# Kernel optimization log

Hardware: AMD Instinct MI355X
Metric: run time of the kernel (lower is better)

## Reference

```python
import jax, jax.numpy as jnp
import numpy as np


def dht(x):
    # Discrete Hartley transform over spatial dims via FFT (ortho norm):
    # H(x) = Re(F(x)) - Im(F(x)). With norm='ortho' the DHT is its own inverse.
    X = jnp.fft.fftn(x, axes=(2, 3), norm='ortho')
    return X.real - X.imag


def _neg_freq(a):
    # H[-k] = roll(flip(H), 1) along both spectral dims
    return jnp.roll(jnp.flip(a, axis=(-2, -1)), shift=(1, 1), axis=(-2, -1))


def compl_mul2d(x1, x2):
    x1n = _neg_freq(x1)
    x2n = _neg_freq(x2)
    return 0.5 * (
        jnp.einsum('bixy,ioxy->boxy', x1, x2)
        - jnp.einsum('bixy,ioxy->boxy', x1n, x2n)
        + jnp.einsum('bixy,ioxy->boxy', x1, x2n)
        + jnp.einsum('bixy,ioxy->boxy', x1n, x2)
    )


def setup_inputs() -> dict:
    key = jax.random.key(0)
    k1, k2 = jax.random.split(key)
    B, Ci, Co, S, M = 16, 32, 32, 256, 16
    x = jax.random.normal(k1, (B, Ci, S, S), dtype=jnp.float32)
    scale = 1.0 / (Ci * Co)
    weights1 = scale * jax.random.uniform(k2, (Ci, Co, M, M), dtype=jnp.float32)
    return {'x': x, 'weights1': weights1}


def reference(x, weights1):
    B = x.shape[0]
    S1, S2 = x.shape[-2], x.shape[-1]
    Co = weights1.shape[1]
    m1, m2 = weights1.shape[2], weights1.shape[3]
    x_ht = dht(x)                                   # [B, Ci, S1, S2]
    res = compl_mul2d(x_ht[:, :, :m1, :m2], weights1)  # [B, Co, m1, m2]
    out_ht = jnp.zeros((B, Co, S1, S2), dtype=x.dtype).at[:, :, :m1, :m2].set(res)
    return dht(out_ht)                              # inverse DHT == DHT (ortho)
```

## Files before the change

kernel.cpp:

```cpp
#include <hip/hip_runtime.h>

#define CI 32
#define CO 32

constexpr float INV_S = 1.0f / 256.0f;
constexpr float THETA = 6.28318530717958647692f / 256.0f;

__device__ constexpr float RC[16] = {
  1.0f,          0.9996988187f, 0.9987954562f, 0.9972904567f,
  0.9951847267f, 0.9924795346f, 0.9891765100f, 0.9852776424f,
  0.9807852804f, 0.9757021300f, 0.9700312532f, 0.9637760658f,
  0.9569403357f, 0.9495281806f, 0.9415440652f, 0.9329927988f};
__device__ constexpr float RS[16] = {
  0.0f,          0.0245412285f, 0.0490676743f, 0.0735645636f,
  0.0980171403f, 0.1224106752f, 0.1467304745f, 0.1709618888f,
  0.1950903220f, 0.2191012402f, 0.2429801799f, 0.2667127575f,
  0.2902846773f, 0.3136817404f, 0.3368898534f, 0.3598950365f};

__global__ __launch_bounds__(256, 2) void k_fwd(const float* __restrict__ x,
                                                float* __restrict__ xh) {
  __shared__ __align__(16) float C1[16][260];
  __shared__ __align__(16) float S1[16][260];
  const int t = threadIdx.x;
  const float* __restrict__ xp = x + (size_t)blockIdx.x * 65536 + t;

  float aC[16], aS[16];
  {
    float x0 = xp[0];
    float xm = xp[128 * 256];
    float e = x0 + xm, o = x0 - xm;
    #pragma unroll
    for (int k = 0; k < 16; ++k) { aC[k] = (k & 1) ? o : e; aS[k] = 0.f; }
  }

  float tc[16], ts[16];
  #pragma unroll
  for (int k = 0; k < 16; ++k) { tc[k] = RC[k]; ts[k] = RS[k]; }

  float xl[8], xhb[8], nxl[8], nxh[8];
  #pragma unroll
  for (int j = 0; j < 8; ++j) {
    xl[j] = xp[(1 + j) * 256];
    xhb[j] = xp[(255 - j) * 256];
  }

  int n0 = 1;
  for (int c = 0; c < 15; ++c, n0 += 8) {
    if (c == 4 || c == 8 || c == 12) {
      #pragma unroll
      for (int k = 0; k < 16; ++k)
        sincosf(THETA * (float)((n0 * k) & 255), &ts[k], &tc[k]);
    }
    if (c < 14) {
      #pragma unroll
      for (int j = 0; j < 8; ++j) {
        nxl[j] = xp[(n0 + 8 + j) * 256];
        nxh[j] = xp[(248 - n0 - j) * 256];
      }
    } else {
      #pragma unroll
      for (int j = 0; j < 7; ++j) {
        nxl[j] = xp[(121 + j) * 256];
        nxh[j] = xp[(135 - j) * 256];
      }
    }
    #pragma unroll
    for (int j = 0; j < 8; ++j) {
      float es = xl[j] + xhb[j];
      float ds = xl[j] - xhb[j];
      #pragma unroll
      for (int k = 0; k < 16; ++k) {
        aC[k] = fmaf(es, tc[k], aC[k]);
        aS[k] = fmaf(ds, ts[k], aS[k]);
        float nc = fmaf(-ts[k], RS[k], tc[k] * RC[k]);
        float ns = fmaf(tc[k], RS[k], ts[k] * RC[k]);
        tc[k] = nc; ts[k] = ns;
      }
    }
    #pragma unroll
    for (int j = 0; j < 8; ++j) { xl[j] = nxl[j]; xhb[j] = nxh[j]; }
  }
  #pragma unroll
  for (int j = 0; j < 7; ++j) {
    float es = xl[j] + xhb[j];
    float ds = xl[j] - xhb[j];
    #pragma unroll
    for (int k = 0; k < 16; ++k) {
      aC[k] = fmaf(es, tc[k], aC[k]);
      aS[k] = fmaf(ds, ts[k], aS[k]);
      float nc = fmaf(-ts[k], RS[k], tc[k] * RC[k]);
      float ns = fmaf(tc[k], RS[k], ts[k] * RC[k]);
      tc[k] = nc; ts[k] = ns;
    }
  }

  #pragma unroll
  for (int k = 0; k < 16; ++k) { C1[k][t] = aC[k]; S1[k][t] = aS[k]; }
  __syncthreads();

  const int k1 = t >> 4, k2 = t & 15;
  float rc2, rs2;
  sincosf(THETA * (float)k2, &rs2, &rc2);
  float acc = 0.f;
  #pragma unroll
  for (int q = 0; q < 4; ++q) {
    const int m = (q * k2) & 3;
    float cc = (m == 0) ? 1.f : (m == 2) ? -1.f : 0.f;
    float ss = (m == 1) ? 1.f : (m == 3) ? -1.f : 0.f;
    #pragma unroll 2
    for (int n2 = q * 64; n2 < q * 64 + 64; n2 += 4) {
      float c4[4], s4[4];
      *(float4*)c4 = *(const float4*)&C1[k1][n2];
      *(float4*)s4 = *(const float4*)&S1[k1][n2];
      #pragma unroll
      for (int jj = 0; jj < 4; ++jj) {
        acc = fmaf(c4[jj], cc + ss, acc);
        acc = fmaf(s4[jj], cc - ss, acc);
        float nc = fmaf(-ss, rs2, cc * rc2);
        float ns = fmaf(cc, rs2, ss * rc2);
        cc = nc; ss = ns;
      }
    }
  }
  xh[(size_t)blockIdx.x * 256 + t] = acc * INV_S;
}

__global__ __launch_bounds__(256, 2) void k_mid(const float* __restrict__ xh,
                                                const float* __restrict__ w,
                                                float* __restrict__ Wout) {
  __shared__ float xs[CI][256];
  __shared__ __align__(16) float rsm[256];
  const int t = threadIdx.x;
  const int b = blockIdx.x >> 5;
  const int o = blockIdx.x & 31;

  #pragma unroll 8
  for (int i = 0; i < CI; ++i)
    xs[i][t] = xh[(size_t)(b * CI + i) * 256 + t];
  __syncthreads();

  const int k1 = t >> 4, k2 = t & 15;
  const int tn = (((16 - k1) & 15) << 4) | ((16 - k2) & 15);
  float acc = 0.f;
  #pragma unroll 8
  for (int i = 0; i < CI; ++i) {
    const float* __restrict__ wrow = w + (size_t)(i * CO + o) * 256;
    float wp = wrow[t];
    float wn = wrow[tn];
    acc = fmaf(xs[i][t], wp + wn, acc);
    acc = fmaf(xs[i][tn], wp - wn, acc);
  }
  rsm[t] = 0.5f * acc;
  __syncthreads();

  const int row = t & 127, h = t >> 7;
  float cc[16], ss[16];
  #pragma unroll
  for (int k = 0; k < 16; ++k)
    sincosf(THETA * (float)((k * row) & 255), &ss[k], &cc[k]);
  float U[8], V[8];
  #pragma unroll
  for (int j = 0; j < 8; ++j) { U[j] = 0.f; V[j] = 0.f; }
  #pragma unroll
  for (int k = 0; k < 16; ++k) {
    float ra[8];
    *(float4*)&ra[0] = *(const float4*)&rsm[k * 16 + 8 * h];
    *(float4*)&ra[4] = *(const float4*)&rsm[k * 16 + 8 * h + 4];
    #pragma unroll
    for (int j = 0; j < 8; ++j) {
      U[j] = fmaf(cc[k], ra[j], U[j]);
      V[j] = fmaf(ss[k], ra[j], V[j]);
    }
  }
  float* __restrict__ wr = Wout + (size_t)blockIdx.x * 4160 + row * 32 + 8 * h;
  {
    float4 u0 = {U[0]*INV_S, U[1]*INV_S, U[2]*INV_S, U[3]*INV_S};
    float4 u1 = {U[4]*INV_S, U[5]*INV_S, U[6]*INV_S, U[7]*INV_S};
    float4 v0 = {V[0]*INV_S, V[1]*INV_S, V[2]*INV_S, V[3]*INV_S};
    float4 v1 = {V[4]*INV_S, V[5]*INV_S, V[6]*INV_S, V[7]*INV_S};
    *(float4*)&wr[0] = u0; *(float4*)&wr[4] = u1;
    *(float4*)&wr[16] = v0; *(float4*)&wr[20] = v1;
  }

  if (row == 0) {
    float U8[8];
    #pragma unroll
    for (int j = 0; j < 8; ++j) U8[j] = 0.f;
    #pragma unroll
    for (int k = 0; k < 16; ++k) {
      float ra[8];
      *(float4*)&ra[0] = *(const float4*)&rsm[k * 16 + 8 * h];
      *(float4*)&ra[4] = *(const float4*)&rsm[k * 16 + 8 * h + 4];
      #pragma unroll
      for (int j = 0; j < 8; ++j)
        U8[j] = (k & 1) ? (U8[j] - ra[j]) : (U8[j] + ra[j]);
    }
    float* __restrict__ wr8 = Wout + (size_t)blockIdx.x * 4160 + 128 * 32 + 8 * h;
    float4 a0 = {U8[0]*INV_S, U8[1]*INV_S, U8[2]*INV_S, U8[3]*INV_S};
    float4 a1 = {U8[4]*INV_S, U8[5]*INV_S, U8[6]*INV_S, U8[7]*INV_S};
    float4 z = {0.f, 0.f, 0.f, 0.f};
    *(float4*)&wr8[0] = a0; *(float4*)&wr8[4] = a1;
    *(float4*)&wr8[16] = z; *(float4*)&wr8[20] = z;
  }
}

__global__ __launch_bounds__(256, 4) void k_invB(const float* __restrict__ Wb,
                                                 float* __restrict__ out) {
  const int t = threadIdx.x;
  const int img = blockIdx.x >> 1;
  const int half = blockIdx.x & 1;

  float cp[16], cm[16];
  #pragma unroll
  for (int k = 0; k < 16; ++k) {
    float s, c;
    sincosf(THETA * (float)((k * t) & 255), &s, &c);
    cp[k] = c + s;
    cm[k] = c - s;
  }

  const float* __restrict__ wbase = Wb + (size_t)img * 4160;
  float* __restrict__ op = out + (size_t)img * 65536 + t;

  const int n_lo = half ? 65 : 0;
  const int n_hi = half ? 128 : 64;
  #pragma unroll 2
  for (int n = n_lo; n <= n_hi; ++n) {
    float uu[16], vv[16];
    #pragma unroll
    for (int q = 0; q < 4; ++q) {
      *(float4*)&uu[4 * q] = *(const float4*)(wbase + n * 32 + 4 * q);
      *(float4*)&vv[4 * q] = *(const float4*)(wbase + n * 32 + 16 + 4 * q);
    }
    float a = 0.f, bsum = 0.f;
    #pragma unroll
    for (int k = 0; k < 16; ++k) {
      a = fmaf(uu[k], cp[k], a);
      bsum = fmaf(vv[k], cm[k], bsum);
    }
    op[(size_t)n * 256] = a + bsum;
    if (n >= 1 && n <= 127) op[(size_t)(256 - n) * 256] = a - bsum;
  }
}

extern "C" void kernel_launch(void* const* d_in, const int* in_sizes, int n_in,
                              void* d_out, int out_size, void* d_ws, size_t ws_size,
                              hipStream_t stream) {
  const float* x = (const float*)d_in[0];
  const float* w = (const float*)d_in[1];
  float* out = (float*)d_out;

  float* xhb = (float*)d_ws;
  float* Wb  = xhb + 131072;

  k_fwd<<<16 * CI, 256, 0, stream>>>(x, xhb);
  k_mid<<<16 * CO, 256, 0, stream>>>(xhb, w, Wb);
  k_invB<<<2 * 16 * CO, 256, 0, stream>>>(Wb, out);
}
```

Baseline: 277.8 us.

## Split forward DHT row sums across two blocks per image and combine partials

The forward kernel now launches two blocks per image, each summing half of the row pairs (1-63 plus the endpoints, and 64-127 with the 128/192 pair) with its own twiddle seeds. Each half writes a partial spectrum, and the mid kernel adds the two partials when loading. This doubles the grid from 512 to 1024 blocks and raises the occupancy hint to 4, aiming to fill more CUs and hide load latency. In exchange the column transform stage runs twice per image and the workspace grows.

```diff
diff --git a/kernel.cpp b/kernel.cpp
--- a/kernel.cpp
+++ b/kernel.cpp
@@ -17,73 +17,19 @@
   0.1950903220f, 0.2191012402f, 0.2429801799f, 0.2667127575f,
   0.2902846773f, 0.3136817404f, 0.3368898534f, 0.3598950365f};
 
-__global__ __launch_bounds__(256, 2) void k_fwd(const float* __restrict__ x,
+__global__ __launch_bounds__(256, 4) void k_fwd(const float* __restrict__ x,
                                                 float* __restrict__ xh) {
   __shared__ __align__(16) float C1[16][260];
   __shared__ __align__(16) float S1[16][260];
   const int t = threadIdx.x;
-  const float* __restrict__ xp = x + (size_t)blockIdx.x * 65536 + t;
-
-  float aC[16], aS[16];
-  {
-    float x0 = xp[0];
-    float xm = xp[128 * 256];
-    float e = x0 + xm, o = x0 - xm;
-    #pragma unroll
-    for (int k = 0; k < 16; ++k) { aC[k] = (k & 1) ? o : e; aS[k] = 0.f; }
-  }
-
-  float tc[16], ts[16];
-  #pragma unroll
-  for (int k = 0; k < 16; ++k) { tc[k] = RC[k]; ts[k] = RS[k]; }
-
-  float xl[8], xhb[8], nxl[8], nxh[8];
-  #pragma unroll
-  for (int j = 0; j < 8; ++j) {
-    xl[j] = xp[(1 + j) * 256];
-    xhb[j] = xp[(255 - j) * 256];
-  }
-
-  int n0 = 1;
-  for (int c = 0; c < 15; ++c, n0 += 8) {
-    if (c == 4 || c == 8 || c == 12) {
-      #pragma unroll
-      for (int k = 0; k < 16; ++k)
-        sincosf(THETA * (float)((n0 * k) & 255), &ts[k], &tc[k]);
-    }
-    if (c < 14) {
-      #pragma unroll
-      for (int j = 0; j < 8; ++j) {
-        nxl[j] = xp[(n0 + 8 + j) * 256];
-        nxh[j] = xp[(248 - n0 - j) * 256];
-      }
-    } else {
-      #pragma unroll
-      for (int j = 0; j < 7; ++j) {
-        nxl[j] = xp[(121 + j) * 256];
-        nxh[j] = xp[(135 - j) * 256];
-      }
-    }
-    #pragma unroll
-    for (int j = 0; j < 8; ++j) {
-      float es = xl[j] + xhb[j];
-      float ds = xl[j] - xhb[j];
-      #pragma unroll
-      for (int k = 0; k < 16; ++k) {
-        aC[k] = fmaf(es, tc[k], aC[k]);
-        aS[k] = fmaf(ds, ts[k], aS[k]);
-        float nc = fmaf(-ts[k], RS[k], tc[k] * RC[k]);
-        float ns = fmaf(tc[k], RS[k], ts[k] * RC[k]);
-        tc[k] = nc; ts[k] = ns;
-      }
-    }
-    #pragma unroll
-    for (int j = 0; j < 8; ++j) { xl[j] = nxl[j]; xhb[j] = nxh[j]; }
-  }
-  #pragma unroll
-  for (int j = 0; j < 7; ++j) {
-    float es = xl[j] + xhb[j];
-    float ds = xl[j] - xhb[j];
+  const int img = blockIdx.x >> 1;
+  const int half = blockIdx.x & 1;
+  const float* __restrict__ xp = x + (size_t)img * 65536 + t;
+
+  float aC[16], aS[16], tc[16], ts[16];
+
+  auto doPair = [&](float lo, float hi) {
+    float es = lo + hi, ds = lo - hi;
     #pragma unroll
     for (int k = 0; k < 16; ++k) {
       aC[k] = fmaf(es, tc[k], aC[k]);
@@ -92,6 +38,67 @@
       float ns = fmaf(tc[k], RS[k], ts[k] * RC[k]);
       tc[k] = nc; ts[k] = ns;
     }
+  };
+
+  const int m0 = half ? 72 : 8;
+  float xl[8], xr[8], nl[8], nr[8];
+
+  if (half == 0) {
+    #pragma unroll
+    for (int j = 0; j < 7; ++j) {
+      xl[j] = xp[(1 + j) * 256];
+      xr[j] = xp[(255 - j) * 256];
+    }
+  } else {
+    #pragma unroll
+    for (int j = 0; j < 8; ++j) {
+      xl[j] = xp[(64 + j) * 256];
+      xr[j] = xp[(192 - j) * 256];
+    }
+  }
+  #pragma unroll
+  for (int j = 0; j < 8; ++j) {
+    nl[j] = xp[(m0 + j) * 256];
+    nr[j] = xp[(256 - m0 - j) * 256];
+  }
+
+  if (half == 0) {
+    #pragma unroll
+    for (int k = 0; k < 16; ++k) { tc[k] = RC[k]; ts[k] = RS[k]; }
+    float x0 = xp[0];
+    float xm = xp[128 * 256];
+    float e = x0 + xm, o = x0 - xm;
+    #pragma unroll
+    for (int k = 0; k < 16; ++k) { aC[k] = (k & 1) ? o : e; aS[k] = 0.f; }
+    #pragma unroll
+    for (int j = 0; j < 7; ++j) doPair(xl[j], xr[j]);
+  } else {
+    #pragma unroll
+    for (int k = 0; k < 16; ++k) {
+      const int m = k & 3;
+      tc[k] = (m == 0) ? 1.f : (m == 2) ? -1.f : 0.f;
+      ts[k] = (m == 1) ? 1.f : (m == 3) ? -1.f : 0.f;
+      aC[k] = 0.f; aS[k] = 0.f;
+    }
+    #pragma unroll
+    for (int j = 0; j < 8; ++j) doPair(xl[j], xr[j]);
+  }
+  #pragma unroll
+  for (int j = 0; j < 8; ++j) { xl[j] = nl[j]; xr[j] = nr[j]; }
+
+  for (int c = 0; c < 7; ++c) {
+    if (c < 6) {
+      const int nx = m0 + 8 * (c + 1);
+      #pragma unroll
+      for (int j = 0; j < 8; ++j) {
+        nl[j] = xp[(nx + j) * 256];
+        nr[j] = xp[(256 - nx - j) * 256];
+      }
+    }
+    #pragma unroll
+    for (int j = 0; j < 8; ++j) doPair(xl[j], xr[j]);
+    #pragma unroll
+    for (int j = 0; j < 8; ++j) { xl[j] = nl[j]; xr[j] = nr[j]; }
   }
 
   #pragma unroll
@@ -122,7 +129,7 @@
       }
     }
   }
-  xh[(size_t)blockIdx.x * 256 + t] = acc * INV_S;
+  xh[(size_t)half * 131072 + (size_t)img * 256 + t] = acc * INV_S;
 }
 
 __global__ __launch_bounds__(256, 2) void k_mid(const float* __restrict__ xh,
@@ -135,8 +142,10 @@
   const int o = blockIdx.x & 31;
 
   #pragma unroll 8
-  for (int i = 0; i < CI; ++i)
-    xs[i][t] = xh[(size_t)(b * CI + i) * 256 + t];
+  for (int i = 0; i < CI; ++i) {
+    const size_t p = (size_t)(b * CI + i) * 256 + t;
+    xs[i][t] = xh[p] + xh[131072 + p];
+  }
   __syncthreads();
 
   const int k1 = t >> 4, k2 = t & 15;
@@ -251,9 +260,9 @@
   float* out = (float*)d_out;
 
   float* xhb = (float*)d_ws;
-  float* Wb  = xhb + 131072;
-
-  k_fwd<<<16 * CI, 256, 0, stream>>>(x, xhb);
+  float* Wb  = xhb + 262144;
+
+  k_fwd<<<2 * 16 * CI, 256, 0, stream>>>(x, xhb);
   k_mid<<<16 * CO, 256, 0, stream>>>(xhb, w, Wb);
   k_invB<<<2 * 16 * CO, 256, 0, stream>>>(Wb, out);
 }
```

After: 419.1 us. 1.51x slower.
